# Optimization experiments

Hardware: AMD Instinct MI355X
Metric: run time of the kernel (lower is better)

Reference implementation:

```python
import jax, jax.numpy as jnp
import numpy as np
import math

B, S, D_MODEL = 4, 2048, 1024
H, D_QK, D_V = 16, 64, 64


def setup_inputs() -> dict:
    key = jax.random.key(0)
    ks = jax.random.split(key, 12)
    s = 0.02
    return {
        "input_q": jax.random.normal(ks[0], (B, S, D_MODEL), jnp.float32),
        "input_k": jax.random.normal(ks[1], (B, S, D_MODEL), jnp.float32),
        "input_v": jax.random.normal(ks[2], (B, S, D_MODEL), jnp.float32),
        # per-head projection weights stacked over heads: [H, out, d_model] (torch Linear layout)
        "WQw": jax.random.normal(ks[3], (H, D_QK, D_MODEL), jnp.float32) * s,
        "WQb": jax.random.normal(ks[4], (H, D_QK), jnp.float32) * s,
        "WKw": jax.random.normal(ks[5], (H, D_QK, D_MODEL), jnp.float32) * s,
        "WKb": jax.random.normal(ks[6], (H, D_QK), jnp.float32) * s,
        "WVw": jax.random.normal(ks[7], (H, D_V, D_MODEL), jnp.float32) * s,
        "WVb": jax.random.normal(ks[8], (H, D_V), jnp.float32) * s,
        # output projection: Linear(H*D_V, D_MODEL)
        "Ww": jax.random.normal(ks[9], (D_MODEL, H * D_V), jnp.float32) * s,
        "Wb": jax.random.normal(ks[10], (D_MODEL,), jnp.float32) * s,
    }


def _mha(input_q, input_k, input_v, WQw, WQb, WKw, WKb, WVw, WVb, Ww, Wb):
    # per-head projections: [B,H,S,d]
    Q = jnp.einsum("bsd,hed->bhse", input_q, WQw) + WQb[None, :, None, :]
    K = jnp.einsum("bsd,hed->bhse", input_k, WKw) + WKb[None, :, None, :]
    V = jnp.einsum("bsd,hvd->bhsv", input_v, WVw) + WVb[None, :, None, :]
    scores = jnp.einsum("bhse,bhte->bhst", Q, K)  # [B,H,S,S]
    # causal mask added BEFORE division by sqrt(d_model), as in original
    causal = jnp.triu(jnp.full((S, S), -jnp.inf, scores.dtype), k=1)
    scores = (scores + causal) / math.sqrt(D_MODEL)  # NOTE: d_model, not d_qk
    attn = jax.nn.softmax(scores, axis=-1)
    ctx = jnp.einsum("bhst,bhtv->bhsv", attn, V)  # [B,H,S,D_V]
    concat = ctx.transpose(0, 2, 1, 3).reshape(B, S, H * D_V)  # head-order concat
    return concat @ Ww.T + Wb


def reference(input_q, input_k, input_v, WQw, WQb, WKw, WKb, WVw, WVb, Ww, Wb):
    return _mha(input_q, input_k, input_v, WQw, WQb, WKw, WKb, WVw, WVb, Ww, Wb)
```

## Files before the change

### kernel.cpp

```cpp
#include <hip/hip_runtime.h>
#include <hip/hip_bf16.h>

typedef __attribute__((ext_vector_type(8))) short bf16x8;
typedef __attribute__((ext_vector_type(4))) short bf16x4;
typedef __attribute__((ext_vector_type(4))) float f32x4;
typedef __attribute__((ext_vector_type(16))) float f32x16;
typedef __attribute__((ext_vector_type(4))) unsigned uint4v;

#define MFMA16(a, b, c) __builtin_amdgcn_mfma_f32_16x16x32_bf16(a, b, c, 0, 0, 0)
#define MFMA32(a, b, c) __builtin_amdgcn_mfma_f32_32x32x16_bf16(a, b, c, 0, 0, 0)

__device__ __forceinline__ unsigned short f2bfn(float f) {
#if defined(__gfx950__)
  __bf16 h = (__bf16)f;
  return __builtin_bit_cast(unsigned short, h);
#else
  union { float f; unsigned u; } x; x.f = f;
  unsigned r = x.u + 0x7fffu + ((x.u >> 16) & 1u);
  return (unsigned short)(r >> 16);
#endif
}

__device__ __forceinline__ void plswap(unsigned& a, unsigned& b) {
  auto r = __builtin_amdgcn_permlane32_swap(a, b, false, false);
  a = r[0];
  b = r[1];
}

__device__ __forceinline__ unsigned cvtpk(float lo, float hi) {
  unsigned w;
  asm("v_cvt_pk_bf16_f32 %0, %1, %2" : "=v"(w) : "v"(lo), "v"(hi));
  return w;
}

__device__ __forceinline__ void cvt_body(const float* __restrict__ s,
                                         unsigned short* __restrict__ d, int n8) {
  int i = blockIdx.x * blockDim.x + threadIdx.x;
  int st = gridDim.x * blockDim.x;
  for (; i < n8; i += st) {
    const float4* sp = reinterpret_cast<const float4*>(s) + 2 * (size_t)i;
    float4 a = sp[0], b = sp[1];
    uint4v o;
    o[0] = cvtpk(a.x, a.y); o[1] = cvtpk(a.z, a.w);
    o[2] = cvtpk(b.x, b.y); o[3] = cvtpk(b.z, b.w);
    reinterpret_cast<uint4v*>(d)[i] = o;
  }
}

__global__ void cvt1_kernel(const float* __restrict__ s, unsigned short* __restrict__ d, int n8) {
  cvt_body(s, d, n8);
}

__global__ void cvt_w_kernel(const float* s0, const float* s1, const float* s2, const float* s3,
                             unsigned short* d0, unsigned short* d1, unsigned short* d2,
                             unsigned short* d3, int n8) {
  const float* s; unsigned short* d;
  switch (blockIdx.y) {
    case 0: s = s0; d = d0; break;
    case 1: s = s1; d = d1; break;
    case 2: s = s2; d = d2; break;
    default: s = s3; d = d3; break;
  }
  cvt_body(s, d, n8);
}

template <int MODE>
__global__ __launch_bounds__(256) void gemm_kernel(
    const unsigned short* __restrict__ Av, const unsigned short* __restrict__ Bv,
    const float* __restrict__ bias, void* __restrict__ outv,
    int M, int N, int K, float oscale) {
  constexpr int BM = 128, BN = 128, BK = 64;
  __shared__ __align__(16) unsigned short As[2][BM * BK];
  __shared__ __align__(16) unsigned short Bs[2][BN * BK];
  const int tid = threadIdx.x;
  const int lane = tid & 63, wave = tid >> 6;
  const int wr = wave >> 1, wc = wave & 1;
  const int m0 = blockIdx.y * BM, n0 = blockIdx.x * BN;
  const int rb = lane & 15, g = lane >> 4;
  const int swz = ((lane & 7) ^ ((lane >> 3) & 7)) * 8;
  f32x4 acc[4][4] = {};

  const unsigned short* Ab = Av + (size_t)m0 * K;
  const unsigned short* Bb = Bv + (size_t)n0 * K;

  auto stage = [&](int buf, int k0) {
#pragma unroll
    for (int i = 0; i < 4; ++i) {
      const int c = wave * 256 + i * 64 + lane;
      const int r = c >> 3;
      __builtin_amdgcn_global_load_lds(
          (const __attribute__((address_space(1))) unsigned int*)(Ab + (size_t)r * K + k0 + swz),
          (__attribute__((address_space(3))) unsigned int*)&As[buf][c * 8], 16, 0, 0);
      __builtin_amdgcn_global_load_lds(
          (const __attribute__((address_space(1))) unsigned int*)(Bb + (size_t)r * K + k0 + swz),
          (__attribute__((address_space(3))) unsigned int*)&Bs[buf][c * 8], 16, 0, 0);
    }
  };

  const int nt = K / BK;
  stage(0, 0);
  int cur = 0;
  for (int t = 0; t < nt; ++t) {
    __syncthreads();
    if (t + 1 < nt) stage(cur ^ 1, (t + 1) * BK);
    const unsigned short* A_ = As[cur];
    const unsigned short* B_ = Bs[cur];
#pragma unroll
    for (int kc = 0; kc < 2; ++kc) {
      bf16x8 af[4], bfr[4];
#pragma unroll
      for (int mi = 0; mi < 4; ++mi)
        af[mi] = *reinterpret_cast<const bf16x8*>(
            &A_[(wr * 64 + mi * 16 + rb) * 64 + (((kc * 4 + g) ^ (rb & 7)) * 8)]);
#pragma unroll
      for (int ni = 0; ni < 4; ++ni)
        bfr[ni] = *reinterpret_cast<const bf16x8*>(
            &B_[(wc * 64 + ni * 16 + rb) * 64 + (((kc * 4 + g) ^ (rb & 7)) * 8)]);
#pragma unroll
      for (int mi = 0; mi < 4; ++mi)
#pragma unroll
        for (int ni = 0; ni < 4; ++ni)
          acc[mi][ni] = MFMA16(af[mi], bfr[ni], acc[mi][ni]);
    }
    cur ^= 1;
  }

#pragma unroll
  for (int mi = 0; mi < 4; ++mi) {
#pragma unroll
    for (int ni = 0; ni < 4; ++ni) {
      int col = n0 + wc * 64 + ni * 16 + rb;
      if constexpr (MODE != 2) {
        float bv = bias[col];
#pragma unroll
        for (int j = 0; j < 4; ++j) {
          int row = m0 + wr * 64 + mi * 16 + g * 4 + j;
          float v = acc[mi][ni][j] + bv;
          if constexpr (MODE == 0) {
            v *= oscale;
            int b = row >> 11, s = row & 2047;
            int h = col >> 6, e = col & 63;
            ((unsigned short*)outv)[((size_t)(b * 16 + h) * 2048 + s) * 64 + e] = f2bfn(v);
          } else {
            ((float*)outv)[(size_t)row * N + col] = v;
          }
        }
      } else {
        int bb = col >> 11, s = col & 2047;
#pragma unroll
        for (int j = 0; j < 4; ++j) {
          int row = m0 + wr * 64 + mi * 16 + g * 4 + j;
          float v = acc[mi][ni][j] + bias[row];
          int h = row >> 6, e = row & 63;
          ((unsigned short*)outv)[((size_t)(bb * 16 + h) * 64 + e) * 2048 + s] = f2bfn(v);
        }
      }
    }
  }
}

__global__ __launch_bounds__(256) void attn6_kernel(
    const unsigned short* __restrict__ Qp, const unsigned short* __restrict__ Kp,
    const unsigned short* __restrict__ Vtp, unsigned short* __restrict__ ctx) {
  constexpr int S = 2048;
  __shared__ __align__(16) unsigned short Ks[2][64 * 64];
  __shared__ __align__(16) unsigned short Vs[2][64 * 64];
  const int bx = blockIdx.x;
  const int bh = bx & 63;
  const int qti = 15 - (bx >> 6);
  const int q0 = qti * 128;
  const int tid = threadIdx.x, wave = tid >> 6, lane = tid & 63;
  const int l31 = lane & 31, hb = lane >> 5, hb4 = hb * 4;
  const int x7 = l31 & 7;
  const int qw = q0 + wave * 32;
  const unsigned short* Qb = Qp + (size_t)bh * S * 64;
  const unsigned short* Kb = Kp + (size_t)bh * S * 64;
  const unsigned short* Vb = Vtp + (size_t)bh * 64 * S;

  bf16x8 qg[4];
#pragma unroll
  for (int kc = 0; kc < 4; ++kc)
    qg[kc] = *reinterpret_cast<const bf16x8*>(
        Qb + (size_t)(qw + l31) * 64 + 16 * kc + 8 * hb);

  bf16x8 ones;
#pragma unroll
  for (int i = 0; i < 8; ++i) ones[i] = (short)0x3F80;

  f32x16 ls = {};
  f32x16 o[2] = {};
  const int sswz = ((lane & 7) ^ (lane >> 3)) * 8;
  const int nt = qti * 2 + 2;

  auto stage = [&](int buf, int kv0) {
#pragma unroll
    for (int i = 0; i < 2; ++i) {
      const int ci = (wave * 2 + i) * 64 + lane;
      const int r = (wave * 2 + i) * 8 + (lane >> 3);
      __builtin_amdgcn_global_load_lds(
          (const __attribute__((address_space(1))) unsigned int*)(Kb + (size_t)(kv0 + r) * 64 + sswz),
          (__attribute__((address_space(3))) unsigned int*)&Ks[buf][ci * 8], 16, 0, 0);
      __builtin_amdgcn_global_load_lds(
          (const __attribute__((address_space(1))) unsigned int*)(Vb + (size_t)r * S + kv0 + sswz),
          (__attribute__((address_space(3))) unsigned int*)&Vs[buf][ci * 8], 16, 0, 0);
    }
  };

  stage(0, 0);

  for (int it = 0; it < nt; ++it) {
    __syncthreads();
    if (it + 1 < nt) stage((it + 1) & 1, 64 * (it + 1));
    const int kv0 = 64 * it;
    if (kv0 <= qw + 31) {
      const unsigned short* K_ = Ks[it & 1];
      const unsigned short* V_ = Vs[it & 1];
      f32x16 sacc[2] = {};
      __builtin_amdgcn_s_setprio(1);
#pragma unroll
      for (int kc = 0; kc < 4; ++kc) {
        bf16x8 kf0 = *reinterpret_cast<const bf16x8*>(
            &K_[l31 * 64 + ((2 * kc + hb) ^ x7) * 8]);
        bf16x8 kf1 = *reinterpret_cast<const bf16x8*>(
            &K_[(32 + l31) * 64 + ((2 * kc + hb) ^ x7) * 8]);
        sacc[0] = MFMA32(kf0, qg[kc], sacc[0]);
        sacc[1] = MFMA32(kf1, qg[kc], sacc[1]);
      }
      __builtin_amdgcn_s_setprio(0);
      if (kv0 + 63 > qw) {
        const int qrel = qw + l31 - kv0;
#pragma unroll
        for (int mi = 0; mi < 2; ++mi)
#pragma unroll
          for (int r = 0; r < 16; ++r) {
            int koff = 32 * mi + (r & 3) + 8 * (r >> 2) + hb4;
            if (koff > qrel) sacc[mi][r] = -1e30f;
          }
      }
      float p0[16], p1[16];
#pragma unroll
      for (int r = 0; r < 16; ++r) p0[r] = __builtin_amdgcn_exp2f(sacc[0][r]);
#pragma unroll
      for (int r = 0; r < 16; ++r) p1[r] = __builtin_amdgcn_exp2f(sacc[1][r]);
      unsigned pw[2][8];
#pragma unroll
      for (int i = 0; i < 8; ++i) pw[0][i] = cvtpk(p0[2 * i], p0[2 * i + 1]);
#pragma unroll
      for (int i = 0; i < 8; ++i) pw[1][i] = cvtpk(p1[2 * i], p1[2 * i + 1]);
#pragma unroll
      for (int mi = 0; mi < 2; ++mi) {
        plswap(pw[mi][0], pw[mi][2]);
        plswap(pw[mi][1], pw[mi][3]);
        plswap(pw[mi][4], pw[mi][6]);
        plswap(pw[mi][5], pw[mi][7]);
      }
      __builtin_amdgcn_s_setprio(1);
#pragma unroll
      for (int c = 0; c < 4; ++c) {
        union { unsigned u[4]; bf16x8 v; } pu;
        pu.u[0] = pw[c >> 1][(c & 1) * 4 + 0];
        pu.u[1] = pw[c >> 1][(c & 1) * 4 + 1];
        pu.u[2] = pw[c >> 1][(c & 1) * 4 + 2];
        pu.u[3] = pw[c >> 1][(c & 1) * 4 + 3];
#pragma unroll
        for (int db = 0; db < 2; ++db) {
          bf16x8 vf = *reinterpret_cast<const bf16x8*>(
              &V_[(32 * db + l31) * 64 + ((2 * c + hb) ^ x7) * 8]);
          o[db] = MFMA32(vf, pu.v, o[db]);
        }
        ls = MFMA32(ones, pu.v, ls);
      }
      __builtin_amdgcn_s_setprio(0);
    }
  }

  const float inv = 1.0f / ls[0];
  const int b = bh >> 4, h = bh & 15;
  const int q = qw + l31;
  unsigned short* cp = ctx + ((size_t)(b * 2048 + q) * 1024) + h * 64;
#pragma unroll
  for (int db = 0; db < 2; ++db)
#pragma unroll
    for (int i = 0; i < 8; ++i) {
      unsigned w = cvtpk(o[db][2 * i] * inv, o[db][2 * i + 1] * inv);
      int d = 32 * db + ((2 * i) & 3) + 8 * (i >> 1) + hb4;
      *reinterpret_cast<unsigned*>(cp + d) = w;
    }
}

extern "C" void kernel_launch(void* const* d_in, const int* in_sizes, int n_in,
                              void* d_out, int out_size, void* d_ws, size_t ws_size,
                              hipStream_t stream) {
  const float* in_q = (const float*)d_in[0];
  const float* in_k = (const float*)d_in[1];
  const float* in_v = (const float*)d_in[2];
  const float* WQw = (const float*)d_in[3];
  const float* WQb = (const float*)d_in[4];
  const float* WKw = (const float*)d_in[5];
  const float* WKb = (const float*)d_in[6];
  const float* WVw = (const float*)d_in[7];
  const float* WVb = (const float*)d_in[8];
  const float* Ww  = (const float*)d_in[9];
  const float* Wb  = (const float*)d_in[10];
  float* out = (float*)d_out;

  constexpr size_t PROJ = (size_t)4 * 16 * 2048 * 64;
  constexpr size_t WSZ = (size_t)1024 * 1024;
  unsigned short* wsp = (unsigned short*)d_ws;
  unsigned short* Qp   = wsp;
  unsigned short* Kp   = wsp + PROJ;
  unsigned short* Vt   = wsp + 2 * PROJ;
  unsigned short* in16 = wsp + 3 * PROJ;
  unsigned short* ctx  = in16;
  unsigned short* wq16 = wsp + 4 * PROJ;
  unsigned short* wk16 = wq16 + WSZ;
  unsigned short* wv16 = wk16 + WSZ;
  unsigned short* ww16 = wv16 + WSZ;

  const float qscale = 0.03125f * 1.4426950408889634f;

  cvt_w_kernel<<<dim3(256, 4), 256, 0, stream>>>(WQw, WKw, WVw, Ww,
                                                 wq16, wk16, wv16, ww16, (int)(WSZ / 8));
  cvt1_kernel<<<2048, 256, 0, stream>>>(in_q, in16, (int)(PROJ / 8));
  gemm_kernel<0><<<dim3(8, 64), 256, 0, stream>>>(in16, wq16, WQb, Qp, 8192, 1024, 1024, qscale);
  cvt1_kernel<<<2048, 256, 0, stream>>>(in_k, in16, (int)(PROJ / 8));
  gemm_kernel<0><<<dim3(8, 64), 256, 0, stream>>>(in16, wk16, WKb, Kp, 8192, 1024, 1024, 1.0f);
  cvt1_kernel<<<2048, 256, 0, stream>>>(in_v, in16, (int)(PROJ / 8));
  gemm_kernel<2><<<dim3(64, 8), 256, 0, stream>>>(wv16, in16, WVb, Vt, 1024, 8192, 1024, 1.0f);

  attn6_kernel<<<1024, 256, 0, stream>>>(Qp, Kp, Vt, ctx);

  gemm_kernel<1><<<dim3(8, 64), 256, 0, stream>>>(ctx, ww16, Wb, out, 8192, 1024, 1024, 1.0f);
}
```

Before: 190.1 us.

## Overlap input conversions with projection GEMMs and drop permlane swaps in attention

Extra thread blocks are appended to the Q and K projection GEMM launches so they convert the next input tensor to bf16 while the GEMM blocks run. Q conversion is merged into the weight conversion launch, and separate bf16 buffers per input are used when the workspace is large enough. In attention, K rows are loaded with a permuted row order so the P fragments line up with the V MFMA operand layout, which removes the permlane32 swaps. The GEMM grid is flattened to 1D, and the overlap path needs a larger workspace and more memory traffic at once.

```diff
diff --git a/kernel.cpp b/kernel.cpp
--- a/kernel.cpp
+++ b/kernel.cpp
@@ -2,7 +2,6 @@
 #include <hip/hip_bf16.h>
 
 typedef __attribute__((ext_vector_type(8))) short bf16x8;
-typedef __attribute__((ext_vector_type(4))) short bf16x4;
 typedef __attribute__((ext_vector_type(4))) float f32x4;
 typedef __attribute__((ext_vector_type(16))) float f32x16;
 typedef __attribute__((ext_vector_type(4))) unsigned uint4v;
@@ -21,22 +20,15 @@
 #endif
 }
 
-__device__ __forceinline__ void plswap(unsigned& a, unsigned& b) {
-  auto r = __builtin_amdgcn_permlane32_swap(a, b, false, false);
-  a = r[0];
-  b = r[1];
-}
-
 __device__ __forceinline__ unsigned cvtpk(float lo, float hi) {
   unsigned w;
   asm("v_cvt_pk_bf16_f32 %0, %1, %2" : "=v"(w) : "v"(lo), "v"(hi));
   return w;
 }
 
-__device__ __forceinline__ void cvt_body(const float* __restrict__ s,
-                                         unsigned short* __restrict__ d, int n8) {
-  int i = blockIdx.x * blockDim.x + threadIdx.x;
-  int st = gridDim.x * blockDim.x;
+__device__ __forceinline__ void cvt_range(const float* __restrict__ s,
+                                          unsigned short* __restrict__ d,
+                                          int i, int st, int n8) {
   for (; i < n8; i += st) {
     const float4* sp = reinterpret_cast<const float4*>(s) + 2 * (size_t)i;
     float4 a = sp[0], b = sp[1];
@@ -48,34 +40,43 @@
 }
 
 __global__ void cvt1_kernel(const float* __restrict__ s, unsigned short* __restrict__ d, int n8) {
-  cvt_body(s, d, n8);
-}
-
-__global__ void cvt_w_kernel(const float* s0, const float* s1, const float* s2, const float* s3,
-                             unsigned short* d0, unsigned short* d1, unsigned short* d2,
-                             unsigned short* d3, int n8) {
-  const float* s; unsigned short* d;
+  cvt_range(s, d, blockIdx.x * blockDim.x + threadIdx.x, gridDim.x * blockDim.x, n8);
+}
+
+__global__ void cvt_first_kernel(const float* s0, const float* s1, const float* s2,
+                                 const float* s3, unsigned short* d0, unsigned short* d1,
+                                 unsigned short* d2, unsigned short* d3, int wn8,
+                                 const float* sq, unsigned short* dq, int qn8) {
+  const float* s; unsigned short* d; int n8;
   switch (blockIdx.y) {
-    case 0: s = s0; d = d0; break;
-    case 1: s = s1; d = d1; break;
-    case 2: s = s2; d = d2; break;
-    default: s = s3; d = d3; break;
-  }
-  cvt_body(s, d, n8);
+    case 0: s = s0; d = d0; n8 = wn8; break;
+    case 1: s = s1; d = d1; n8 = wn8; break;
+    case 2: s = s2; d = d2; n8 = wn8; break;
+    case 3: s = s3; d = d3; n8 = wn8; break;
+    default: s = sq; d = dq; n8 = qn8; break;
+  }
+  cvt_range(s, d, blockIdx.x * blockDim.x + threadIdx.x, gridDim.x * blockDim.x, n8);
 }
 
 template <int MODE>
 __global__ __launch_bounds__(256) void gemm_kernel(
     const unsigned short* __restrict__ Av, const unsigned short* __restrict__ Bv,
     const float* __restrict__ bias, void* __restrict__ outv,
-    int M, int N, int K, float oscale) {
+    int M, int N, int K, float oscale, int nshift, int ngemm,
+    const float* __restrict__ csrc, unsigned short* __restrict__ cdst, int cn8) {
   constexpr int BM = 128, BN = 128, BK = 64;
   __shared__ __align__(16) unsigned short As[2][BM * BK];
   __shared__ __align__(16) unsigned short Bs[2][BN * BK];
+  const int bx = blockIdx.x;
   const int tid = threadIdx.x;
+  if (bx >= ngemm) {
+    cvt_range(csrc, cdst, (bx - ngemm) * blockDim.x + tid,
+              (gridDim.x - ngemm) * blockDim.x, cn8);
+    return;
+  }
   const int lane = tid & 63, wave = tid >> 6;
   const int wr = wave >> 1, wc = wave & 1;
-  const int m0 = blockIdx.y * BM, n0 = blockIdx.x * BN;
+  const int m0 = (bx >> nshift) * BM, n0 = (bx & ((1 << nshift) - 1)) * BN;
   const int rb = lane & 15, g = lane >> 4;
   const int swz = ((lane & 7) ^ ((lane >> 3) & 7)) * 8;
   f32x4 acc[4][4] = {};
@@ -159,7 +160,7 @@
   }
 }
 
-__global__ __launch_bounds__(256) void attn6_kernel(
+__global__ __launch_bounds__(256) void attn7_kernel(
     const unsigned short* __restrict__ Qp, const unsigned short* __restrict__ Kp,
     const unsigned short* __restrict__ Vtp, unsigned short* __restrict__ ctx) {
   constexpr int S = 2048;
@@ -168,11 +169,10 @@
   const int bx = blockIdx.x;
   const int bh = bx & 63;
   const int qti = 15 - (bx >> 6);
-  const int q0 = qti * 128;
   const int tid = threadIdx.x, wave = tid >> 6, lane = tid & 63;
-  const int l31 = lane & 31, hb = lane >> 5, hb4 = hb * 4;
+  const int l31 = lane & 31, hb = lane >> 5;
   const int x7 = l31 & 7;
-  const int qw = q0 + wave * 32;
+  const int qw = qti * 128 + wave * 32;
   const unsigned short* Qb = Qp + (size_t)bh * S * 64;
   const unsigned short* Kb = Kp + (size_t)bh * S * 64;
   const unsigned short* Vb = Vtp + (size_t)bh * 64 * S;
@@ -192,25 +192,37 @@
   const int sswz = ((lane & 7) ^ (lane >> 3)) * 8;
   const int nt = qti * 2 + 2;
 
-  auto stage = [&](int buf, int kv0) {
-#pragma unroll
-    for (int i = 0; i < 2; ++i) {
-      const int ci = (wave * 2 + i) * 64 + lane;
-      const int r = (wave * 2 + i) * 8 + (lane >> 3);
-      __builtin_amdgcn_global_load_lds(
-          (const __attribute__((address_space(1))) unsigned int*)(Kb + (size_t)(kv0 + r) * 64 + sswz),
-          (__attribute__((address_space(3))) unsigned int*)&Ks[buf][ci * 8], 16, 0, 0);
-      __builtin_amdgcn_global_load_lds(
-          (const __attribute__((address_space(1))) unsigned int*)(Vb + (size_t)r * S + kv0 + sswz),
-          (__attribute__((address_space(3))) unsigned int*)&Vs[buf][ci * 8], 16, 0, 0);
-    }
+  const int ci0 = wave * 2 * 64 + lane, ci1 = ci0 + 64;
+  const int r0 = wave * 16 + (lane >> 3), r1 = r0 + 8;
+  const int rs0 = (r0 & 51) | ((r0 & 4) << 1) | ((r0 & 8) >> 1);
+  const int rs1 = (r1 & 51) | ((r1 & 4) << 1) | ((r1 & 8) >> 1);
+  const unsigned short* ks0 = Kb + (size_t)rs0 * 64 + sswz;
+  const unsigned short* ks1 = Kb + (size_t)rs1 * 64 + sswz;
+  const unsigned short* vs0 = Vb + (size_t)r0 * S + sswz;
+  const unsigned short* vs1 = Vb + (size_t)r1 * S + sswz;
+
+  auto stage = [&](int buf) {
+    __builtin_amdgcn_global_load_lds(
+        (const __attribute__((address_space(1))) unsigned int*)ks0,
+        (__attribute__((address_space(3))) unsigned int*)&Ks[buf][ci0 * 8], 16, 0, 0);
+    __builtin_amdgcn_global_load_lds(
+        (const __attribute__((address_space(1))) unsigned int*)ks1,
+        (__attribute__((address_space(3))) unsigned int*)&Ks[buf][ci1 * 8], 16, 0, 0);
+    __builtin_amdgcn_global_load_lds(
+        (const __attribute__((address_space(1))) unsigned int*)vs0,
+        (__attribute__((address_space(3))) unsigned int*)&Vs[buf][ci0 * 8], 16, 0, 0);
+    __builtin_amdgcn_global_load_lds(
+        (const __attribute__((address_space(1))) unsigned int*)vs1,
+        (__attribute__((address_space(3))) unsigned int*)&Vs[buf][ci1 * 8], 16, 0, 0);
+    ks0 += 4096; ks1 += 4096;
+    vs0 += 64; vs1 += 64;
   };
 
-  stage(0, 0);
+  stage(0);
 
   for (int it = 0; it < nt; ++it) {
     __syncthreads();
-    if (it + 1 < nt) stage((it + 1) & 1, 64 * (it + 1));
+    if (it + 1 < nt) stage((it + 1) & 1);
     const int kv0 = 64 * it;
     if (kv0 <= qw + 31) {
       const unsigned short* K_ = Ks[it & 1];
@@ -228,12 +240,12 @@
       }
       __builtin_amdgcn_s_setprio(0);
       if (kv0 + 63 > qw) {
-        const int qrel = qw + l31 - kv0;
+        const int qrel = qw + l31 - kv0 - 8 * hb;
 #pragma unroll
         for (int mi = 0; mi < 2; ++mi)
 #pragma unroll
           for (int r = 0; r < 16; ++r) {
-            int koff = 32 * mi + (r & 3) + 8 * (r >> 2) + hb4;
+            int koff = (r & 7) + 16 * (r >> 3) + 32 * mi;
             if (koff > qrel) sacc[mi][r] = -1e30f;
           }
       }
@@ -247,13 +259,6 @@
       for (int i = 0; i < 8; ++i) pw[0][i] = cvtpk(p0[2 * i], p0[2 * i + 1]);
 #pragma unroll
       for (int i = 0; i < 8; ++i) pw[1][i] = cvtpk(p1[2 * i], p1[2 * i + 1]);
-#pragma unroll
-      for (int mi = 0; mi < 2; ++mi) {
-        plswap(pw[mi][0], pw[mi][2]);
-        plswap(pw[mi][1], pw[mi][3]);
-        plswap(pw[mi][4], pw[mi][6]);
-        plswap(pw[mi][5], pw[mi][7]);
-      }
       __builtin_amdgcn_s_setprio(1);
 #pragma unroll
       for (int c = 0; c < 4; ++c) {
@@ -283,7 +288,7 @@
 #pragma unroll
     for (int i = 0; i < 8; ++i) {
       unsigned w = cvtpk(o[db][2 * i] * inv, o[db][2 * i + 1] * inv);
-      int d = 32 * db + ((2 * i) & 3) + 8 * (i >> 1) + hb4;
+      int d = 32 * db + ((2 * i) & 3) + 8 * (i >> 1) + 4 * hb;
       *reinterpret_cast<unsigned*>(cp + d) = w;
     }
 }
@@ -306,29 +311,60 @@
 
   constexpr size_t PROJ = (size_t)4 * 16 * 2048 * 64;
   constexpr size_t WSZ = (size_t)1024 * 1024;
+  const float qscale = 0.03125f * 1.4426950408889634f;
   unsigned short* wsp = (unsigned short*)d_ws;
-  unsigned short* Qp   = wsp;
-  unsigned short* Kp   = wsp + PROJ;
-  unsigned short* Vt   = wsp + 2 * PROJ;
-  unsigned short* in16 = wsp + 3 * PROJ;
-  unsigned short* ctx  = in16;
-  unsigned short* wq16 = wsp + 4 * PROJ;
-  unsigned short* wk16 = wq16 + WSZ;
-  unsigned short* wv16 = wk16 + WSZ;
-  unsigned short* ww16 = wv16 + WSZ;
-
-  const float qscale = 0.03125f * 1.4426950408889634f;
-
-  cvt_w_kernel<<<dim3(256, 4), 256, 0, stream>>>(WQw, WKw, WVw, Ww,
-                                                 wq16, wk16, wv16, ww16, (int)(WSZ / 8));
-  cvt1_kernel<<<2048, 256, 0, stream>>>(in_q, in16, (int)(PROJ / 8));
-  gemm_kernel<0><<<dim3(8, 64), 256, 0, stream>>>(in16, wq16, WQb, Qp, 8192, 1024, 1024, qscale);
-  cvt1_kernel<<<2048, 256, 0, stream>>>(in_k, in16, (int)(PROJ / 8));
-  gemm_kernel<0><<<dim3(8, 64), 256, 0, stream>>>(in16, wk16, WKb, Kp, 8192, 1024, 1024, 1.0f);
-  cvt1_kernel<<<2048, 256, 0, stream>>>(in_v, in16, (int)(PROJ / 8));
-  gemm_kernel<2><<<dim3(64, 8), 256, 0, stream>>>(wv16, in16, WVb, Vt, 1024, 8192, 1024, 1.0f);
-
-  attn6_kernel<<<1024, 256, 0, stream>>>(Qp, Kp, Vt, ctx);
-
-  gemm_kernel<1><<<dim3(8, 64), 256, 0, stream>>>(ctx, ww16, Wb, out, 8192, 1024, 1024, 1.0f);
-}
+
+  const bool fused = ws_size >= (6 * PROJ + 4 * WSZ) * sizeof(unsigned short);
+
+  if (fused) {
+    unsigned short* Qp   = wsp;
+    unsigned short* Kp   = wsp + PROJ;
+    unsigned short* Vt   = wsp + 2 * PROJ;
+    unsigned short* inq  = wsp + 3 * PROJ;
+    unsigned short* ctx  = inq;
+    unsigned short* ink  = wsp + 4 * PROJ;
+    unsigned short* inv  = wsp + 5 * PROJ;
+    unsigned short* wq16 = wsp + 6 * PROJ;
+    unsigned short* wk16 = wq16 + WSZ;
+    unsigned short* wv16 = wk16 + WSZ;
+    unsigned short* ww16 = wv16 + WSZ;
+
+    cvt_first_kernel<<<dim3(1024, 5), 256, 0, stream>>>(
+        WQw, WKw, WVw, Ww, wq16, wk16, wv16, ww16, (int)(WSZ / 8),
+        in_q, inq, (int)(PROJ / 8));
+    gemm_kernel<0><<<2560, 256, 0, stream>>>(inq, wq16, WQb, Qp, 8192, 1024, 1024,
+                                             qscale, 3, 512, in_k, ink, (int)(PROJ / 8));
+    gemm_kernel<0><<<2560, 256, 0, stream>>>(ink, wk16, WKb, Kp, 8192, 1024, 1024,
+                                             1.0f, 3, 512, in_v, inv, (int)(PROJ / 8));
+    gemm_kernel<2><<<512, 256, 0, stream>>>(wv16, inv, WVb, Vt, 1024, 8192, 1024,
+                                            1.0f, 6, 512, nullptr, nullptr, 0);
+    attn7_kernel<<<1024, 256, 0, stream>>>(Qp, Kp, Vt, ctx);
+    gemm_kernel<1><<<512, 256, 0, stream>>>(ctx, ww16, Wb, out, 8192, 1024, 1024,
+                                            1.0f, 3, 512, nullptr, nullptr, 0);
+  } else {
+    unsigned short* Qp   = wsp;
+    unsigned short* Kp   = wsp + PROJ;
+    unsigned short* Vt   = wsp + 2 * PROJ;
+    unsigned short* in16 = wsp + 3 * PROJ;
+    unsigned short* ctx  = in16;
+    unsigned short* wq16 = wsp + 4 * PROJ;
+    unsigned short* wk16 = wq16 + WSZ;
+    unsigned short* wv16 = wk16 + WSZ;
+    unsigned short* ww16 = wv16 + WSZ;
+
+    cvt_first_kernel<<<dim3(1024, 5), 256, 0, stream>>>(
+        WQw, WKw, WVw, Ww, wq16, wk16, wv16, ww16, (int)(WSZ / 8),
+        in_q, in16, (int)(PROJ / 8));
+    gemm_kernel<0><<<512, 256, 0, stream>>>(in16, wq16, WQb, Qp, 8192, 1024, 1024,
+                                            qscale, 3, 512, nullptr, nullptr, 0);
+    cvt1_kernel<<<2048, 256, 0, stream>>>(in_k, in16, (int)(PROJ / 8));
+    gemm_kernel<0><<<512, 256, 0, stream>>>(in16, wk16, WKb, Kp, 8192, 1024, 1024,
+                                            1.0f, 3, 512, nullptr, nullptr, 0);
+    cvt1_kernel<<<2048, 256, 0, stream>>>(in_v, in16, (int)(PROJ / 8));
+    gemm_kernel<2><<<512, 256, 0, stream>>>(wv16, in16, WVb, Vt, 1024, 8192, 1024,
+                                            1.0f, 6, 512, nullptr, nullptr, 0);
+    attn7_kernel<<<1024, 256, 0, stream>>>(Qp, Kp, Vt, ctx);
+    gemm_kernel<1><<<512, 256, 0, stream>>>(ctx, ww16, Wb, out, 8192, 1024, 1024,
+                                            1.0f, 3, 512, nullptr, nullptr, 0);
+  }
+}
```

New measurement: 184.0 us. 1.03x faster.
